# Optimization experiments

Hardware: AMD Instinct MI355X
Metric: run time of the kernel (lower is better)

The kernel has to match this reference:

```python
import itertools
import jax, jax.numpy as jnp
import numpy as np
from jax import lax

INT_STEPS = 7
DOWN = 2


def _sample(vol, coords):
    """Trilinear sample vol [C, D, H, W] at voxel coords [3, D2, H2, W2].
    Matches torch grid_sample(align_corners=True, padding_mode='zeros') after
    voxelmorph's voxel->[-1,1] normalization (i.e. plain voxel coordinates)."""
    dims = vol.shape[1:]
    c0f = jnp.floor(coords)
    frac = coords - c0f
    c0 = c0f.astype(jnp.int32)
    out = jnp.zeros((vol.shape[0],) + coords.shape[1:], vol.dtype)
    for corner in itertools.product((0, 1), repeat=3):
        w = jnp.ones(coords.shape[1:], vol.dtype)
        valid = True
        idxs = []
        for ax in range(3):
            idx = c0[ax] + corner[ax]
            w = w * (frac[ax] if corner[ax] else 1.0 - frac[ax])
            valid = valid & (idx >= 0) & (idx < dims[ax])
            idxs.append(jnp.clip(idx, 0, dims[ax] - 1))
        out = out + vol[:, idxs[0], idxs[1], idxs[2]] * (w * valid)
    return out


def _grid(shape, dtype):
    return jnp.stack(jnp.meshgrid(*[jnp.arange(s, dtype=dtype) for s in shape], indexing='ij'))


def _warp(src, flow):
    # SpatialTransformer: sample src at identity grid + flow (voxel coords)
    return _sample(src, _grid(src.shape[1:], flow.dtype) + flow)


def _resize(x, out_shape):
    # F.interpolate trilinear, align_corners=True: src = i*(in-1)/(out-1)
    coords = jnp.stack(jnp.meshgrid(
        *[jnp.linspace(0.0, s_in - 1.0, s_out, dtype=x.dtype)
          for s_in, s_out in zip(x.shape[1:], out_shape)], indexing='ij'))
    return _sample(x, coords)


def _flow_single(pos_flow, label):
    # pos_flow: [3, D, H, W], label: [1, D, H, W]
    full = pos_flow.shape[1:]
    down_shape = tuple(s // DOWN for s in full)
    # ResizeTransform(int_downsize): factor=1/DOWN<1 -> resize then scale
    f = _resize(pos_flow, down_shape) * (1.0 / DOWN)
    # VecInt: scaling and squaring
    f = f * (1.0 / (2 ** INT_STEPS))
    for _ in range(INT_STEPS):
        f = f + _warp(f, f)
    # ResizeTransform(1/int_downsize): factor=DOWN>1 -> scale then resize
    f = _resize(f * float(DOWN), full)
    moved = _warp(label, f)
    return moved, f


def setup_inputs() -> dict:
    key = jax.random.key(0)
    k1, k2, k3 = jax.random.split(key, 3)
    B, F, D, H, W = 1, 16, 128, 128, 128
    features = jax.random.normal(k1, (B, F, D, H, W), jnp.float32)
    moving_label = jax.random.uniform(k2, (B, 1, D, H, W), jnp.float32)
    # conv weight initialized Normal(0, 1e-5), bias zeros (as in module)
    weight = jax.random.normal(k3, (3, F, 3, 3, 3), jnp.float32) * 1e-5
    bias = jnp.zeros((3,), jnp.float32)
    return {"features": features, "moving_label": moving_label,
            "weight": weight, "bias": bias}


def reference(features, moving_label, weight, bias):
    pos_flow = lax.conv_general_dilated(
        features, weight, window_strides=(1, 1, 1),
        padding=[(1, 1)] * 3,
        dimension_numbers=('NCDHW', 'OIDHW', 'NCDHW'))
    pos_flow = pos_flow + bias[None, :, None, None, None]
    moved, flow = jax.vmap(_flow_single)(pos_flow, moving_label)
    return moved, flow
```

## Files before the change

### kernel.cpp

```cpp
#include <hip/hip_runtime.h>


#define V128 2097152
#define V64  262144

typedef __attribute__((ext_vector_type(2))) float f32x2;
typedef float f32x2u __attribute__((ext_vector_type(2), aligned(4)));

template <int C>
__device__ __forceinline__ void trisample(const float* __restrict__ vol,
                                          int D, int H, int W, int cstride,
                                          float cz, float cy, float cx,
                                          float* out) {
    float fz = floorf(cz), fy = floorf(cy), fx = floorf(cx);
    int iz = (int)fz, iy = (int)fy, ix = (int)fx;
    float tz = cz - fz, ty = cy - fy, tx = cx - fx;
#pragma unroll
    for (int c = 0; c < C; ++c) out[c] = 0.0f;
#pragma unroll
    for (int dz = 0; dz < 2; ++dz) {
#pragma unroll
        for (int dy = 0; dy < 2; ++dy) {
#pragma unroll
            for (int dx = 0; dx < 2; ++dx) {
                int z = iz + dz, y = iy + dy, x = ix + dx;
                float w = (dz ? tz : 1.0f - tz) *
                          (dy ? ty : 1.0f - ty) *
                          (dx ? tx : 1.0f - tx);
                bool valid = (z >= 0) && (z < D) && (y >= 0) && (y < H) &&
                             (x >= 0) && (x < W);
                int zc = min(max(z, 0), D - 1);
                int yc = min(max(y, 0), H - 1);
                int xc = min(max(x, 0), W - 1);
                int base = (zc * H + yc) * W + xc;
                float wv = valid ? w : 0.0f;
#pragma unroll
                for (int c = 0; c < C; ++c)
                    out[c] += vol[c * cstride + base] * wv;
            }
        }
    }
}

template <int SI>
__device__ __forceinline__ void lds_lerp3(const float* __restrict__ f,
                                          float pz, float py, float px,
                                          float* out) {
    constexpr int NI = SI * SI * SI;
    float fz = floorf(pz), fy = floorf(py), fx = floorf(px);
    int iz = (int)fz, iy = (int)fy, ix = (int)fx;
    float tz = pz - fz, ty = py - fy, tx = px - fx;
    int b = (iz * SI + iy) * SI + ix;
    float wz0 = 1.0f - tz, wy0 = 1.0f - ty, wx0 = 1.0f - tx;
#pragma unroll
    for (int c = 0; c < 3; ++c) {
        const float* fc = f + c * NI;
        float v00 = fc[b] * wx0 + fc[b + 1] * tx;
        float v01 = fc[b + SI] * wx0 + fc[b + SI + 1] * tx;
        float v10 = fc[b + SI * SI] * wx0 + fc[b + SI * SI + 1] * tx;
        float v11 = fc[b + SI * SI + SI] * wx0 + fc[b + SI * SI + SI + 1] * tx;
        out[c] = wz0 * (wy0 * v00 + ty * v01) + tz * (wy0 * v10 + ty * v11);
    }
}

template <int SI, int NT>
__device__ __forceinline__ void step_lds(const float* __restrict__ in,
                                         float* __restrict__ out, int tid) {
    constexpr int SO = SI - 2;
    constexpr int NI = SI * SI * SI;
    constexpr int NO = SO * SO * SO;
    for (int i = tid; i < NO; i += NT) {
        int xx = i % SO, yy = (i / SO) % SO, zz = i / (SO * SO);
        int la = ((zz + 1) * SI + (yy + 1)) * SI + (xx + 1);
        float fz = in[la], fy = in[la + NI], fx = in[la + 2 * NI];
        float sm[3];
        lds_lerp3<SI>(in, (zz + 1) + fz, (yy + 1) + fy, (xx + 1) + fx, sm);
        out[i] = fz + sm[0];
        out[i + NO] = fy + sm[1];
        out[i + 2 * NO] = fx + sm[2];
    }
}

template <int NT>
__device__ __forceinline__ void step_to_global(const float* __restrict__ in,
                                               float* __restrict__ gout,
                                               int tx, int ty, int tz,
                                               int tid) {
    constexpr int SI = 10;
    constexpr int NI = SI * SI * SI;
    for (int i = tid; i < 512; i += NT) {
        int xx = i & 7, yy = (i >> 3) & 7, zz = i >> 6;
        int la = ((zz + 1) * SI + (yy + 1)) * SI + (xx + 1);
        float fz = in[la], fy = in[la + NI], fx = in[la + 2 * NI];
        float sm[3];
        lds_lerp3<SI>(in, (zz + 1) + fz, (yy + 1) + fy, (xx + 1) + fx, sm);
        int n3 = ((((tz + zz) << 12) + ((ty + yy) << 6) + (tx + xx))) * 3;
        gout[n3] = fz + sm[0];
        gout[n3 + 1] = fy + sm[1];
        gout[n3 + 2] = fx + sm[2];
    }
}

__global__ __launch_bounds__(256) void conv_kernel(
    const float* __restrict__ feat, const float* __restrict__ weight,
    const float* __restrict__ bias, float* __restrict__ pf) {
    __shared__ float smem[2][4356];
    const int tid = threadIdx.x;
    const int x0 = blockIdx.x * 64, y0 = blockIdx.y * 4, z0 = blockIdx.z * 8;
    const int lx = tid & 63, ly = tid >> 6;

    int goff[16];
    int laddr[16];
    unsigned vmask = 0;
#pragma unroll
    for (int k = 0; k < 16; ++k) {
        int s = tid + 256 * k;
        int xx = s % 66;
        int r = s / 66;
        int yy = r % 6;
        int zz = r / 6;
        laddr[k] = (yy * 66 + xx) * 11 + zz;
        bool intile = (k < 15) || (tid < 120);
        int gx = x0 + xx - 1, gy = y0 + yy - 1, gz = z0 + zz - 1;
        bool ok = intile && ((unsigned)gx < 128u) && ((unsigned)gy < 128u) &&
                  ((unsigned)gz < 128u);
        goff[k] = (gz << 14) + (gy << 7) + gx;
        if (ok) vmask |= (1u << k);
    }

    f32x2 acc[3][4];
#pragma unroll
    for (int o = 0; o < 3; ++o)
#pragma unroll
        for (int zp = 0; zp < 4; ++zp) acc[o][zp] = (f32x2)(0.0f);

    {
        float vals[16];
#pragma unroll
        for (int k = 0; k < 16; ++k) {
            vals[k] = 0.0f;
            if (vmask & (1u << k)) vals[k] = feat[goff[k]];
        }
#pragma unroll
        for (int k = 0; k < 16; ++k)
            if (k < 15 || tid < 120) smem[0][laddr[k]] = vals[k];
    }

    for (int c = 0; c < 16; ++c) {
        __syncthreads();
        if (c + 1 < 16) {
            const float* fc = feat + ((c + 1) << 21);
            float* buf = smem[(c + 1) & 1];
            float vals[16];
#pragma unroll
            for (int k = 0; k < 16; ++k) {
                vals[k] = 0.0f;
                if (vmask & (1u << k)) vals[k] = fc[goff[k]];
            }
#pragma unroll
            for (int k = 0; k < 16; ++k)
                if (k < 15 || tid < 120) buf[laddr[k]] = vals[k];
        }
        const float* buf = smem[c & 1];
        const float* wc = weight + c * 27;
#pragma unroll
        for (int dy = 0; dy < 3; ++dy) {
#pragma unroll
            for (int dx = 0; dx < 3; ++dx) {
                const float* p = buf + ((ly + dy) * 66 + lx + dx) * 11;
                f32x2 pv[5];
                f32x2 qv[4];
#pragma unroll
                for (int k2 = 0; k2 < 5; ++k2)
                    pv[k2] = *(const f32x2u*)(p + 2 * k2);
#pragma unroll
                for (int k2 = 0; k2 < 4; ++k2)
                    qv[k2] = *(const f32x2u*)(p + 2 * k2 + 1);
#pragma unroll
                for (int o = 0; o < 3; ++o) {
                    float w0 = wc[o * 432 + 0 + dy * 3 + dx];
                    float w1 = wc[o * 432 + 9 + dy * 3 + dx];
                    float w2 = wc[o * 432 + 18 + dy * 3 + dx];
#pragma unroll
                    for (int zp = 0; zp < 4; ++zp) {
                        acc[o][zp] += pv[zp] * (f32x2)(w0);
                        acc[o][zp] += qv[zp] * (f32x2)(w1);
                        acc[o][zp] += pv[zp + 1] * (f32x2)(w2);
                    }
                }
            }
        }
    }

    float b0 = bias[0], b1 = bias[1], b2 = bias[2];
#pragma unroll
    for (int zp = 0; zp < 4; ++zp) {
        int vox0 = ((z0 + 2 * zp) << 14) + ((y0 + ly) << 7) + x0 + lx;
#pragma unroll
        for (int h = 0; h < 2; ++h) {
            int m3 = (vox0 + (h << 14)) * 3;
            pf[m3] = (h ? acc[0][zp].y : acc[0][zp].x) + b0;
            pf[m3 + 1] = (h ? acc[1][zp].y : acc[1][zp].x) + b1;
            pf[m3 + 2] = (h ? acc[2][zp].y : acc[2][zp].x) + b2;
        }
    }
}

__global__ __launch_bounds__(256) void ds_kernel(const float* __restrict__ pf,
                                                 float* __restrict__ dsf) {
    int i = blockIdx.x * 256 + threadIdx.x;
    int gx = i & 63, gy = (i >> 6) & 63, gz = i >> 12;
    const float s2 = 127.0f / 63.0f;
    const float k = 1.0f / 256.0f;
    float cz = gz * s2, cy = gy * s2, cx = gx * s2;
    int iz = min((int)cz, 126);
    int iy = min((int)cy, 126);
    int ix = min((int)cx, 126);
    float tzf = cz - (float)iz;
    float tyf = cy - (float)iy;
    float txf = cx - (float)ix;
    float wz[2] = {1.0f - tzf, tzf};
    float wy[2] = {1.0f - tyf, tyf};
    float wx[2] = {1.0f - txf, txf};
    int b = ((iz << 14) + (iy << 7) + ix) * 3;
    float v0 = 0.0f, v1 = 0.0f, v2 = 0.0f;
#pragma unroll
    for (int dz = 0; dz < 2; ++dz)
#pragma unroll
        for (int dy = 0; dy < 2; ++dy)
#pragma unroll
            for (int dx = 0; dx < 2; ++dx) {
                float w = wz[dz] * wy[dy] * wx[dx];
                int bb = b + dz * (3 << 14) + dy * (3 << 7) + dx * 3;
                v0 += pf[bb] * w;
                v1 += pf[bb + 1] * w;
                v2 += pf[bb + 2] * w;
            }
    int o3 = i * 3;
    dsf[o3] = v0 * k;
    dsf[o3 + 1] = v1 * k;
    dsf[o3 + 2] = v2 * k;
}

__global__ __launch_bounds__(512) void f23_kernel(
    const float* __restrict__ gin, float* __restrict__ gout) {
    __shared__ float A[3 * 2744];
    __shared__ float B[3 * 1728];
    const int tid = threadIdx.x;
    const int tx = blockIdx.x * 8, ty = blockIdx.y * 8, tz = blockIdx.z * 8;
    const int rbx = tx - 3, rby = ty - 3, rbz = tz - 3;
    for (int i = tid; i < 2744; i += 512) {
        int xx = i % 14, yy = (i / 14) % 14, zz = i / 196;
        int gz = rbz + zz, gy = rby + yy, gx = rbx + xx;
        float v0 = 0.0f, v1 = 0.0f, v2 = 0.0f;
        if ((unsigned)gz < 64u && (unsigned)gy < 64u && (unsigned)gx < 64u) {
            int n3 = ((gz << 12) + (gy << 6) + gx) * 3;
            v0 = gin[n3];
            v1 = gin[n3 + 1];
            v2 = gin[n3 + 2];
        }
        A[i] = v0;
        A[i + 2744] = v1;
        A[i + 2 * 2744] = v2;
    }
    __syncthreads();
    step_lds<14, 512>(A, B, tid);
    __syncthreads();
    step_lds<12, 512>(B, A, tid);
    __syncthreads();
    step_to_global<512>(A, gout, tx, ty, tz, tid);
}

__global__ __launch_bounds__(512) void f4_kernel(
    const float* __restrict__ gin, const float* __restrict__ label,
    float* __restrict__ moved, float* __restrict__ flow) {
    __shared__ float A[3 * 2197];
    __shared__ float B[3 * 1331];
    const int tid = threadIdx.x;
    const int ttx = blockIdx.x, tty = blockIdx.y, ttz = blockIdx.z;
    const int r0x = (1008 * ttx) / 127 - 1;
    const int r0y = (1008 * tty) / 127 - 1;
    const int r0z = (1008 * ttz) / 127 - 1;
    const int rbx = r0x - 1, rby = r0y - 1, rbz = r0z - 1;
    for (int i = tid; i < 2197; i += 512) {
        int xx = i % 13, yy = (i / 13) % 13, zz = i / 169;
        int gz = rbz + zz, gy = rby + yy, gx = rbx + xx;
        float v0 = 0.0f, v1 = 0.0f, v2 = 0.0f;
        if ((unsigned)gz < 64u && (unsigned)gy < 64u && (unsigned)gx < 64u) {
            int n3 = ((gz << 12) + (gy << 6) + gx) * 3;
            v0 = gin[n3];
            v1 = gin[n3 + 1];
            v2 = gin[n3 + 2];
        }
        A[i] = v0;
        A[i + 2197] = v1;
        A[i + 2 * 2197] = v2;
    }
    __syncthreads();
    step_lds<13, 512>(A, B, tid);
    __syncthreads();
    const float s3 = 63.0f / 127.0f;
    for (int i = tid; i < 4096; i += 512) {
        int lx = i & 15, ly = (i >> 4) & 15, lz = i >> 8;
        int gx = ttx * 16 + lx, gy = tty * 16 + ly, gz = ttz * 16 + lz;
        float f[3];
        lds_lerp3<11>(B, gz * s3 - (float)r0z, gy * s3 - (float)r0y,
                      gx * s3 - (float)r0x, f);
        float fz = 2.0f * f[0], fy = 2.0f * f[1], fx = 2.0f * f[2];
        int m = (gz << 14) + (gy << 7) + gx;
        flow[m] = fz;
        flow[m + V128] = fy;
        flow[m + 2 * V128] = fx;
        float mv[1];
        trisample<1>(label, 128, 128, 128, 0, gz + fz, gy + fy, gx + fx, mv);
        moved[m] = mv[0];
    }
}

extern "C" void kernel_launch(void* const* d_in, const int* in_sizes, int n_in,
                              void* d_out, int out_size, void* d_ws,
                              size_t ws_size, hipStream_t stream) {
    const float* features = (const float*)d_in[0];
    const float* label = (const float*)d_in[1];
    const float* weight = (const float*)d_in[2];
    const float* bias = (const float*)d_in[3];
    float* out = (float*)d_out;
    float* moved = out;
    float* flow = out + V128;
    float* dsf = moved;
    float* fA = (float*)d_ws;
    float* fB = fA + 3 * V64;

    conv_kernel<<<dim3(2, 32, 16), 256, 0, stream>>>(features, weight, bias,
                                                     flow);
    ds_kernel<<<dim3(1024), 256, 0, stream>>>(flow, dsf);
    f23_kernel<<<dim3(8, 8, 8), 512, 0, stream>>>(dsf, fA);
    f23_kernel<<<dim3(8, 8, 8), 512, 0, stream>>>(fA, fB);
    f4_kernel<<<dim3(8, 8, 8), 512, 0, stream>>>(fB, label, moved, flow);
}
```

Before: 292.5 us.

## Fuse downsample into first integration kernel and merge last four steps with upsample

The downsample pass now runs inside the first squaring kernel's halo load, and the second squaring kernel is merged with the final upsample/warp kernel. That kernel does four LDS-resident integration steps on a larger 19^3 halo tile. Two launches and the global round trips of intermediate flow fields go away. In exchange there is more redundant halo recomputation, and LDS use per block grows to about 140KB, which may cut occupancy to one block per CU.

```diff
diff --git a/kernel.cpp b/kernel.cpp
--- a/kernel.cpp
+++ b/kernel.cpp
@@ -206,51 +206,69 @@
     }
 }
 
-__global__ __launch_bounds__(256) void ds_kernel(const float* __restrict__ pf,
-                                                 float* __restrict__ dsf) {
-    int i = blockIdx.x * 256 + threadIdx.x;
-    int gx = i & 63, gy = (i >> 6) & 63, gz = i >> 12;
-    const float s2 = 127.0f / 63.0f;
-    const float k = 1.0f / 256.0f;
-    float cz = gz * s2, cy = gy * s2, cx = gx * s2;
-    int iz = min((int)cz, 126);
-    int iy = min((int)cy, 126);
-    int ix = min((int)cx, 126);
-    float tzf = cz - (float)iz;
-    float tyf = cy - (float)iy;
-    float txf = cx - (float)ix;
-    float wz[2] = {1.0f - tzf, tzf};
-    float wy[2] = {1.0f - tyf, tyf};
-    float wx[2] = {1.0f - txf, txf};
-    int b = ((iz << 14) + (iy << 7) + ix) * 3;
-    float v0 = 0.0f, v1 = 0.0f, v2 = 0.0f;
-#pragma unroll
-    for (int dz = 0; dz < 2; ++dz)
-#pragma unroll
-        for (int dy = 0; dy < 2; ++dy)
-#pragma unroll
-            for (int dx = 0; dx < 2; ++dx) {
-                float w = wz[dz] * wy[dy] * wx[dx];
-                int bb = b + dz * (3 << 14) + dy * (3 << 7) + dx * 3;
-                v0 += pf[bb] * w;
-                v1 += pf[bb + 1] * w;
-                v2 += pf[bb + 2] * w;
-            }
-    int o3 = i * 3;
-    dsf[o3] = v0 * k;
-    dsf[o3 + 1] = v1 * k;
-    dsf[o3 + 2] = v2 * k;
-}
-
-__global__ __launch_bounds__(512) void f23_kernel(
-    const float* __restrict__ gin, float* __restrict__ gout) {
+__global__ __launch_bounds__(512) void f2b_kernel(
+    const float* __restrict__ pf, float* __restrict__ gout) {
     __shared__ float A[3 * 2744];
     __shared__ float B[3 * 1728];
     const int tid = threadIdx.x;
     const int tx = blockIdx.x * 8, ty = blockIdx.y * 8, tz = blockIdx.z * 8;
     const int rbx = tx - 3, rby = ty - 3, rbz = tz - 3;
+    const float s2 = 127.0f / 63.0f;
+    const float k = 1.0f / 256.0f;
     for (int i = tid; i < 2744; i += 512) {
         int xx = i % 14, yy = (i / 14) % 14, zz = i / 196;
+        int gz = rbz + zz, gy = rby + yy, gx = rbx + xx;
+        float v0 = 0.0f, v1 = 0.0f, v2 = 0.0f;
+        if ((unsigned)gz < 64u && (unsigned)gy < 64u && (unsigned)gx < 64u) {
+            float cz = gz * s2, cy = gy * s2, cx = gx * s2;
+            int iz = min((int)cz, 126);
+            int iy = min((int)cy, 126);
+            int ix = min((int)cx, 126);
+            float tzf = cz - (float)iz;
+            float tyf = cy - (float)iy;
+            float txf = cx - (float)ix;
+            float wz[2] = {1.0f - tzf, tzf};
+            float wy[2] = {1.0f - tyf, tyf};
+            float wx[2] = {1.0f - txf, txf};
+            int b = ((iz << 14) + (iy << 7) + ix) * 3;
+#pragma unroll
+            for (int dz = 0; dz < 2; ++dz)
+#pragma unroll
+                for (int dy = 0; dy < 2; ++dy)
+#pragma unroll
+                    for (int dx = 0; dx < 2; ++dx) {
+                        float w = wz[dz] * wy[dy] * wx[dx];
+                        int bb = b + dz * (3 << 14) + dy * (3 << 7) + dx * 3;
+                        v0 += pf[bb] * w;
+                        v1 += pf[bb + 1] * w;
+                        v2 += pf[bb + 2] * w;
+                    }
+        }
+        A[i] = v0 * k;
+        A[i + 2744] = v1 * k;
+        A[i + 2 * 2744] = v2 * k;
+    }
+    __syncthreads();
+    step_lds<14, 512>(A, B, tid);
+    __syncthreads();
+    step_lds<12, 512>(B, A, tid);
+    __syncthreads();
+    step_to_global<512>(A, gout, tx, ty, tz, tid);
+}
+
+__global__ __launch_bounds__(512) void f47_kernel(
+    const float* __restrict__ gin, const float* __restrict__ label,
+    float* __restrict__ moved, float* __restrict__ flow) {
+    __shared__ float A[3 * 6859];
+    __shared__ float B[3 * 4913];
+    const int tid = threadIdx.x;
+    const int ttx = blockIdx.x, tty = blockIdx.y, ttz = blockIdx.z;
+    const int r0x = (1008 * ttx) / 127 - 1;
+    const int r0y = (1008 * tty) / 127 - 1;
+    const int r0z = (1008 * ttz) / 127 - 1;
+    const int rbx = r0x - 4, rby = r0y - 4, rbz = r0z - 4;
+    for (int i = tid; i < 6859; i += 512) {
+        int xx = i % 19, yy = (i / 19) % 19, zz = i / 361;
         int gz = rbz + zz, gy = rby + yy, gx = rbx + xx;
         float v0 = 0.0f, v1 = 0.0f, v2 = 0.0f;
         if ((unsigned)gz < 64u && (unsigned)gy < 64u && (unsigned)gx < 64u) {
@@ -260,51 +278,24 @@
             v2 = gin[n3 + 2];
         }
         A[i] = v0;
-        A[i + 2744] = v1;
-        A[i + 2 * 2744] = v2;
-    }
-    __syncthreads();
-    step_lds<14, 512>(A, B, tid);
-    __syncthreads();
-    step_lds<12, 512>(B, A, tid);
-    __syncthreads();
-    step_to_global<512>(A, gout, tx, ty, tz, tid);
-}
-
-__global__ __launch_bounds__(512) void f4_kernel(
-    const float* __restrict__ gin, const float* __restrict__ label,
-    float* __restrict__ moved, float* __restrict__ flow) {
-    __shared__ float A[3 * 2197];
-    __shared__ float B[3 * 1331];
-    const int tid = threadIdx.x;
-    const int ttx = blockIdx.x, tty = blockIdx.y, ttz = blockIdx.z;
-    const int r0x = (1008 * ttx) / 127 - 1;
-    const int r0y = (1008 * tty) / 127 - 1;
-    const int r0z = (1008 * ttz) / 127 - 1;
-    const int rbx = r0x - 1, rby = r0y - 1, rbz = r0z - 1;
-    for (int i = tid; i < 2197; i += 512) {
-        int xx = i % 13, yy = (i / 13) % 13, zz = i / 169;
-        int gz = rbz + zz, gy = rby + yy, gx = rbx + xx;
-        float v0 = 0.0f, v1 = 0.0f, v2 = 0.0f;
-        if ((unsigned)gz < 64u && (unsigned)gy < 64u && (unsigned)gx < 64u) {
-            int n3 = ((gz << 12) + (gy << 6) + gx) * 3;
-            v0 = gin[n3];
-            v1 = gin[n3 + 1];
-            v2 = gin[n3 + 2];
-        }
-        A[i] = v0;
-        A[i + 2197] = v1;
-        A[i + 2 * 2197] = v2;
-    }
-    __syncthreads();
-    step_lds<13, 512>(A, B, tid);
+        A[i + 6859] = v1;
+        A[i + 2 * 6859] = v2;
+    }
+    __syncthreads();
+    step_lds<19, 512>(A, B, tid);
+    __syncthreads();
+    step_lds<17, 512>(B, A, tid);
+    __syncthreads();
+    step_lds<15, 512>(A, B, tid);
+    __syncthreads();
+    step_lds<13, 512>(B, A, tid);
     __syncthreads();
     const float s3 = 63.0f / 127.0f;
     for (int i = tid; i < 4096; i += 512) {
         int lx = i & 15, ly = (i >> 4) & 15, lz = i >> 8;
         int gx = ttx * 16 + lx, gy = tty * 16 + ly, gz = ttz * 16 + lz;
         float f[3];
-        lds_lerp3<11>(B, gz * s3 - (float)r0z, gy * s3 - (float)r0y,
+        lds_lerp3<11>(A, gz * s3 - (float)r0z, gy * s3 - (float)r0y,
                       gx * s3 - (float)r0x, f);
         float fz = 2.0f * f[0], fy = 2.0f * f[1], fx = 2.0f * f[2];
         int m = (gz << 14) + (gy << 7) + gx;
@@ -327,14 +318,10 @@
     float* out = (float*)d_out;
     float* moved = out;
     float* flow = out + V128;
-    float* dsf = moved;
     float* fA = (float*)d_ws;
-    float* fB = fA + 3 * V64;
 
     conv_kernel<<<dim3(2, 32, 16), 256, 0, stream>>>(features, weight, bias,
                                                      flow);
-    ds_kernel<<<dim3(1024), 256, 0, stream>>>(flow, dsf);
-    f23_kernel<<<dim3(8, 8, 8), 512, 0, stream>>>(dsf, fA);
-    f23_kernel<<<dim3(8, 8, 8), 512, 0, stream>>>(fA, fB);
-    f4_kernel<<<dim3(8, 8, 8), 512, 0, stream>>>(fB, label, moved, flow);
-}
+    f2b_kernel<<<dim3(8, 8, 8), 512, 0, stream>>>(flow, fA);
+    f47_kernel<<<dim3(8, 8, 8), 512, 0, stream>>>(fA, label, moved, flow);
+}
```

New measurement: 314.9 us. 7.7% more time.
